# Kernel tuning notes

Measured on AMD Instinct MI355X. Metric: run time of the kernel, lower is better.

## Reference

```python
import jax, jax.numpy as jnp
import numpy as np

DIM = 1024
NUM_HEADS = 16
MASKED = True


def setup_inputs() -> dict:
    key = jax.random.key(0)
    ks = jax.random.split(key, 9)
    B, S, D = 2, 2048, DIM
    return {
        "x": jax.random.normal(ks[0], (B, S, D), dtype=jnp.float32),
        "Wq": jax.random.normal(ks[1], (D, D), dtype=jnp.float32),
        "bq": jax.random.normal(ks[2], (D,), dtype=jnp.float32),
        "Wk": jax.random.normal(ks[3], (D, D), dtype=jnp.float32),
        "bk": jax.random.normal(ks[4], (D,), dtype=jnp.float32),
        "Wv": jax.random.normal(ks[5], (D, D), dtype=jnp.float32),
        "bv": jax.random.normal(ks[6], (D,), dtype=jnp.float32),
        "Wo": jax.random.normal(ks[7], (D, D), dtype=jnp.float32),
        "bo": jax.random.normal(ks[8], (D,), dtype=jnp.float32),
    }


def _mha(x, Wq, bq, Wk, bk, Wv, bv, Wo, bo):
    B, S, D = x.shape
    H = NUM_HEADS
    hd = D // H
    # projections (torch Linear stores [out,in]; here W is [out,in], x @ W.T + b)
    q = x @ Wq.T + bq
    k = x @ Wk.T + bk
    v = x @ Wv.T + bv
    # [B, H, S, hd]
    q = q.reshape(B, S, H, hd).transpose(0, 2, 1, 3)
    k = k.reshape(B, S, H, hd).transpose(0, 2, 1, 3)
    v = v.reshape(B, S, H, hd).transpose(0, 2, 1, 3)
    scores = jnp.einsum("bhqd,bhkd->bhqk", q, k) / jnp.sqrt(jnp.asarray(hd, x.dtype))
    if MASKED:
        mask = jnp.tril(jnp.ones((S, S), dtype=bool))
        scores = jnp.where(mask, scores, -jnp.inf)
    attn = jax.nn.softmax(scores, axis=-1)
    out = jnp.einsum("bhqk,bhkd->bhqd", attn, v)
    out = out.transpose(0, 2, 1, 3).reshape(B, S, D)
    return out @ Wo.T + bo


def reference(x, Wq, bq, Wk, bk, Wv, bv, Wo, bo):
    return _mha(x, Wq, bq, Wk, bk, Wv, bv, Wo, bo)
```

## Files before the change

### kernel.cpp

```cpp
#include <hip/hip_runtime.h>

typedef unsigned short u16;
typedef unsigned int u32;
typedef __attribute__((ext_vector_type(4))) float f32x4;
typedef __attribute__((ext_vector_type(8))) __bf16 bf16x8;

#define L2E 1.4426950408889634f

__device__ __forceinline__ u16 f2bf(float f) { return __builtin_bit_cast(u16, (__bf16)f); }
__device__ __forceinline__ float bf2f(u16 h) { return (float)__builtin_bit_cast(__bf16, h); }
__device__ __forceinline__ f32x4 mfma16(bf16x8 a, bf16x8 b, f32x4 c) {
  return __builtin_amdgcn_mfma_f32_16x16x32_bf16(a, b, c, 0, 0, 0);
}
__device__ __forceinline__ void gl_lds16(const u16* g, u16* l) {
  __builtin_amdgcn_global_load_lds((__attribute__((address_space(1))) void*)g,
                                   (__attribute__((address_space(3))) void*)l,
                                   16, 0, 0);
}
__device__ __forceinline__ f32x4 fzero() {
  f32x4 v = {0.f, 0.f, 0.f, 0.f};
  return v;
}

__global__ void k_prep(const float* __restrict__ x, const float* __restrict__ Wq,
                       const float* __restrict__ Wk, const float* __restrict__ Wv,
                       const float* __restrict__ Wo,
                       u16* __restrict__ xh, u16* __restrict__ xl,
                       u16* __restrict__ wqh, u16* __restrict__ wql,
                       u16* __restrict__ wkh, u16* __restrict__ wkl,
                       u16* __restrict__ wvb, u16* __restrict__ wob) {
  int i = (blockIdx.x * 256 + threadIdx.x) * 4;
  const float* src;
  u16* hi;
  u16* lo;
  int j;
  if (i < 4194304)      { src = x;  hi = xh;  lo = xl;      j = i; }
  else if (i < 5242880) { src = Wq; hi = wqh; lo = wql;     j = i - 4194304; }
  else if (i < 6291456) { src = Wk; hi = wkh; lo = wkl;     j = i - 5242880; }
  else if (i < 7340032) { src = Wv; hi = wvb; lo = nullptr; j = i - 6291456; }
  else                  { src = Wo; hi = wob; lo = nullptr; j = i - 7340032; }
  float4 v = *(const float4*)(src + j);
  float vv[4] = {v.x, v.y, v.z, v.w};
  u16 hh[4];
#pragma unroll
  for (int t = 0; t < 4; ++t) hh[t] = f2bf(vv[t]);
  *(ushort4*)(hi + j) = make_ushort4(hh[0], hh[1], hh[2], hh[3]);
  if (lo) {
    u16 ll[4];
#pragma unroll
    for (int t = 0; t < 4; ++t) ll[t] = f2bf(vv[t] - bf2f(hh[t]));
    *(ushort4*)(lo + j) = make_ushort4(ll[0], ll[1], ll[2], ll[3]);
  }
}

template <int SPLIT, int EPI>
__device__ __forceinline__ void gemm_body(
    u16* sm, const u16* __restrict__ Ah, const u16* __restrict__ Al,
    const u16* __restrict__ Bh, const u16* __restrict__ Bl,
    const float* __restrict__ bias, float scale,
    u16* __restrict__ oH, u16* __restrict__ oL, float* __restrict__ oF,
    int m0, int n0) {
  u16* sAh = sm;
  u16* sBh = sm + 4096;
  u16* sAl = SPLIT ? (sm + 8192) : sm;
  u16* sBl = SPLIT ? (sm + 12288) : sm;

  const int tid = threadIdx.x;
  const int lane = tid & 63, w = tid >> 6;
  const int wm = w >> 1, wn = w & 1;
  const int fr = lane & 15, fg = lane >> 4;
  const int srow = tid >> 2, scb = (tid & 3) * 8;

  f32x4 acc[4][4];
#pragma unroll
  for (int i = 0; i < 4; ++i)
#pragma unroll
    for (int j = 0; j < 4; ++j) acc[i][j] = fzero();

  for (int kk = 0; kk < 1024; kk += 32) {
    __syncthreads();
#pragma unroll
    for (int r = 0; r < 2; ++r) {
      int row = r * 64 + srow;
      gl_lds16(Ah + (size_t)(m0 + row) * 1024 + kk + scb, sAh + row * 32 + scb);
      gl_lds16(Bh + (size_t)(n0 + row) * 1024 + kk + scb, sBh + row * 32 + scb);
      if constexpr (SPLIT) {
        gl_lds16(Al + (size_t)(m0 + row) * 1024 + kk + scb, sAl + row * 32 + scb);
        gl_lds16(Bl + (size_t)(n0 + row) * 1024 + kk + scb, sBl + row * 32 + scb);
      }
    }
    __syncthreads();

    bf16x8 ah[4], bh[4], al[4], bl[4];
#pragma unroll
    for (int i = 0; i < 4; ++i) {
      ah[i] = *(const bf16x8*)(sAh + (wm * 64 + i * 16 + fr) * 32 + fg * 8);
      bh[i] = *(const bf16x8*)(sBh + (wn * 64 + i * 16 + fr) * 32 + fg * 8);
      if constexpr (SPLIT) {
        al[i] = *(const bf16x8*)(sAl + (wm * 64 + i * 16 + fr) * 32 + fg * 8);
        bl[i] = *(const bf16x8*)(sBl + (wn * 64 + i * 16 + fr) * 32 + fg * 8);
      }
    }
#pragma unroll
    for (int i = 0; i < 4; ++i)
#pragma unroll
      for (int j = 0; j < 4; ++j) {
        acc[i][j] = mfma16(ah[i], bh[j], acc[i][j]);
        if constexpr (SPLIT) {
          acc[i][j] = mfma16(ah[i], bl[j], acc[i][j]);
          acc[i][j] = mfma16(al[i], bh[j], acc[i][j]);
        }
      }
  }

#pragma unroll
  for (int i = 0; i < 4; ++i)
#pragma unroll
    for (int j = 0; j < 4; ++j) {
      int cg = n0 + wn * 64 + j * 16 + fr;
      float bv = bias[cg];
#pragma unroll
      for (int r = 0; r < 4; ++r) {
        int rg = m0 + wm * 64 + i * 16 + fg * 4 + r;
        float val = (acc[i][j][r] + bv) * scale;
        if constexpr (EPI == 0) {
          int b = rg >> 11, s = rg & 2047, hd2 = cg >> 6, dd = cg & 63;
          size_t off = ((size_t)((b * 16 + hd2) * 2048 + s)) * 64 + dd;
          u16 hv = f2bf(val);
          oH[off] = hv;
          oL[off] = f2bf(val - bf2f(hv));
        } else if constexpr (EPI == 1) {
          int b = rg >> 11, s = rg & 2047, hd2 = cg >> 6, dd = cg & 63;
          size_t off = ((size_t)((b * 16 + hd2) * 64 + dd)) * 2048 + s;
          oH[off] = f2bf(val);
        } else {
          oF[(size_t)rg * 1024 + cg] = val;
        }
      }
    }
}

__global__ __launch_bounds__(256) void k_qkv(
    const u16* __restrict__ xh, const u16* __restrict__ xl,
    const u16* __restrict__ wqh, const u16* __restrict__ wql,
    const u16* __restrict__ wkh, const u16* __restrict__ wkl,
    const u16* __restrict__ wvb,
    const float* __restrict__ bq, const float* __restrict__ bk,
    const float* __restrict__ bv,
    u16* __restrict__ qh, u16* __restrict__ ql,
    u16* __restrict__ kh, u16* __restrict__ kl, u16* __restrict__ vt) {
  __shared__ u16 sm[16384];
  int which = blockIdx.y >> 3;
  int m0 = blockIdx.x * 128, n0 = (blockIdx.y & 7) * 128;
  if (which == 0)
    gemm_body<1, 0>(sm, xh, xl, wqh, wql, bq, 0.125f * L2E, qh, ql, nullptr, m0, n0);
  else if (which == 1)
    gemm_body<1, 0>(sm, xh, xl, wkh, wkl, bk, 1.0f, kh, kl, nullptr, m0, n0);
  else
    gemm_body<0, 1>(sm, xh, nullptr, wvb, nullptr, bv, 1.0f, vt, nullptr, nullptr, m0, n0);
}

__global__ __launch_bounds__(256) void k_oproj(
    const u16* __restrict__ ao, const u16* __restrict__ wob,
    const float* __restrict__ bo, float* __restrict__ out) {
  __shared__ u16 sm[8192];
  gemm_body<0, 2>(sm, ao, nullptr, wob, nullptr, bo, 1.0f, nullptr, nullptr, out,
                  blockIdx.x * 128, blockIdx.y * 128);
}

__global__ __launch_bounds__(256) void k_attn(
    const u16* __restrict__ Qh, const u16* __restrict__ Ql,
    const u16* __restrict__ Kh, const u16* __restrict__ Kl,
    const u16* __restrict__ Vt, u16* __restrict__ Oa) {
  __shared__ u16 sKh[2][4096], sKl[2][4096], sVt[2][4096];
  __shared__ u16 sP[4][1024];

  const int tid = threadIdx.x;
  const int lane = tid & 63, w = tid >> 6;
  const int fr = lane & 15, fg = lane >> 4;

  const int d = blockIdx.x;
  const int bh = (d & 7) * 4 + (d >> 7);
  const int pr = (d >> 3) & 15;

  const size_t base = (size_t)bh * 131072;
  const u16* Qh_p = Qh + base;
  const u16* Ql_p = Ql + base;
  const u16* Kh_p = Kh + base;
  const u16* Kl_p = Kl + base;
  const u16* Vt_p = Vt + base;
  const int bb = bh >> 4, hh = bh & 15;

  const int srow8 = tid >> 3, scb8 = tid & 7;

  auto STAGE = [&](int t, int c) {
#pragma unroll
    for (int r2 = 0; r2 < 2; ++r2) {
      int row = r2 * 32 + srow8;
      int cbs = scb8 ^ (row & 7);
      gl_lds16(Kh_p + ((size_t)(t * 64 + row)) * 64 + cbs * 8, &sKh[c][row * 64 + scb8 * 8]);
      gl_lds16(Kl_p + ((size_t)(t * 64 + row)) * 64 + cbs * 8, &sKl[c][row * 64 + scb8 * 8]);
      gl_lds16(Vt_p + (size_t)row * 2048 + t * 64 + cbs * 8, &sVt[c][row * 64 + scb8 * 8]);
    }
  };

  for (int half = 0; half < 2; ++half) {
    const int j = half ? (31 - pr) : pr;
    const int nt = j + 1;
    const int qrow = j * 64 + w * 16 + fr;

    bf16x8 qhf[2], qlf[2];
#pragma unroll
    for (int ks = 0; ks < 2; ++ks) {
      qhf[ks] = *(const bf16x8*)(Qh_p + (size_t)qrow * 64 + ks * 32 + fg * 8);
      qlf[ks] = *(const bf16x8*)(Ql_p + (size_t)qrow * 64 + ks * 32 + fg * 8);
    }

    float mx = -1e30f, l = 0.f;
    f32x4 o[4];
#pragma unroll
    for (int f = 0; f < 4; ++f) o[f] = fzero();

    STAGE(0, 0);

    for (int t = 0; t < nt; ++t) {
      const int cur = t & 1;
      if (t + 1 < nt) {
        STAGE(t + 1, cur ^ 1);
        asm volatile("s_waitcnt vmcnt(6)" ::: "memory");
      } else {
        asm volatile("s_waitcnt vmcnt(0)" ::: "memory");
      }
      asm volatile("s_barrier" ::: "memory");

      const u16* kbh = sKh[cur];
      const u16* kbl = sKl[cur];
      const u16* vbb = sVt[cur];

      f32x4 sc[4];
      __builtin_amdgcn_s_setprio(1);
#pragma unroll
      for (int f = 0; f < 4; ++f) {
        f32x4 a = fzero();
#pragma unroll
        for (int ks = 0; ks < 2; ++ks) {
          int row = f * 16 + fr;
          int cb = (fg + 4 * ks) ^ (fr & 7);
          bf16x8 khv = *(const bf16x8*)(kbh + row * 64 + cb * 8);
          bf16x8 klv = *(const bf16x8*)(kbl + row * 64 + cb * 8);
          a = mfma16(khv, qhf[ks], a);
          a = mfma16(khv, qlf[ks], a);
          a = mfma16(klv, qhf[ks], a);
        }
        sc[f] = a;
      }
      __builtin_amdgcn_s_setprio(0);

      if (t == nt - 1) {
#pragma unroll
        for (int f = 0; f < 4; ++f)
#pragma unroll
          for (int r = 0; r < 4; ++r) {
            int kvg = t * 64 + f * 16 + fg * 4 + r;
            if (kvg > qrow) sc[f][r] = -1e30f;
          }
      }

      float pm = -1e30f;
#pragma unroll
      for (int f = 0; f < 4; ++f)
#pragma unroll
        for (int r = 0; r < 4; ++r) pm = fmaxf(pm, sc[f][r]);
      pm = fmaxf(pm, __shfl_xor(pm, 16, 64));
      pm = fmaxf(pm, __shfl_xor(pm, 32, 64));

      const bool resc = __any(pm > mx + 11.5f);
      float alp = 1.0f;
      if (resc) {
        float mn = fmaxf(mx, pm);
        alp = exp2f(mx - mn);
        mx = mn;
      }

      float ps = 0.f;
#pragma unroll
      for (int f = 0; f < 4; ++f) {
        float p0 = exp2f(sc[f][0] - mx);
        float p1 = exp2f(sc[f][1] - mx);
        float p2 = exp2f(sc[f][2] - mx);
        float p3 = exp2f(sc[f][3] - mx);
        ps += (p0 + p1) + (p2 + p3);
        uint2 pv;
        pv.x = (u32)f2bf(p0) | ((u32)f2bf(p1) << 16);
        pv.y = (u32)f2bf(p2) | ((u32)f2bf(p3) << 16);
        int e = (f * 16 + fg * 4) ^ ((fr & 7) << 3);
        *(uint2*)(&sP[w][fr * 64 + e]) = pv;
      }
      ps += __shfl_xor(ps, 16, 64);
      ps += __shfl_xor(ps, 32, 64);
      l = l * alp + ps;

      if (resc) {
        float alpb[4];
#pragma unroll
        for (int r = 0; r < 4; ++r) alpb[r] = __shfl(alp, fg * 4 + r, 64);
#pragma unroll
        for (int f = 0; f < 4; ++f)
#pragma unroll
          for (int r = 0; r < 4; ++r) o[f][r] *= alpb[r];
      }

      __builtin_amdgcn_s_setprio(1);
#pragma unroll
      for (int ks = 0; ks < 2; ++ks) {
        int e = (ks * 32 + fg * 8) ^ ((fr & 7) << 3);
        bf16x8 pa = *(const bf16x8*)(&sP[w][fr * 64 + e]);
#pragma unroll
        for (int f = 0; f < 4; ++f) {
          int row = f * 16 + fr;
          int cb = (fg + 4 * ks) ^ (fr & 7);
          bf16x8 vb = *(const bf16x8*)(vbb + row * 64 + cb * 8);
          o[f] = mfma16(pa, vb, o[f]);
        }
      }
      __builtin_amdgcn_s_setprio(0);

      asm volatile("s_barrier" ::: "memory");
    }

    float lb[4];
#pragma unroll
    for (int r = 0; r < 4; ++r) lb[r] = __shfl(l, fg * 4 + r, 64);
#pragma unroll
    for (int f = 0; f < 4; ++f)
#pragma unroll
      for (int r = 0; r < 4; ++r) {
        int qg = j * 64 + w * 16 + fg * 4 + r;
        float val = o[f][r] / lb[r];
        Oa[((size_t)(bb * 2048 + qg)) * 1024 + hh * 64 + f * 16 + fr] = f2bf(val);
      }
  }
}

extern "C" void kernel_launch(void* const* d_in, const int* in_sizes, int n_in,
                              void* d_out, int out_size, void* d_ws, size_t ws_size,
                              hipStream_t stream) {
  const float* x  = (const float*)d_in[0];
  const float* Wq = (const float*)d_in[1];
  const float* bq = (const float*)d_in[2];
  const float* Wk = (const float*)d_in[3];
  const float* bk = (const float*)d_in[4];
  const float* Wv = (const float*)d_in[5];
  const float* bv = (const float*)d_in[6];
  const float* Wo = (const float*)d_in[7];
  const float* bo = (const float*)d_in[8];
  float* out = (float*)d_out;

  u16* ws  = (u16*)d_ws;
  u16* xh  = ws;
  u16* xl  = xh + 4194304;
  u16* wqh = xl + 4194304;
  u16* wql = wqh + 1048576;
  u16* wkh = wql + 1048576;
  u16* wkl = wkh + 1048576;
  u16* wvb = wkl + 1048576;
  u16* wob = wvb + 1048576;
  u16* qh  = wob + 1048576;
  u16* ql  = qh + 4194304;
  u16* kh  = ql + 4194304;
  u16* kl  = kh + 4194304;
  u16* vt  = kl + 4194304;
  u16* ao  = xh;

  k_prep<<<8192, 256, 0, stream>>>(x, Wq, Wk, Wv, Wo, xh, xl, wqh, wql, wkh, wkl, wvb, wob);
  k_qkv<<<dim3(32, 24), 256, 0, stream>>>(xh, xl, wqh, wql, wkh, wkl, wvb, bq, bk, bv,
                                          qh, ql, kh, kl, vt);
  k_attn<<<512, 256, 0, stream>>>(qh, ql, kh, kl, vt, ao);
  k_oproj<<<dim3(32, 8), 256, 0, stream>>>(ao, wob, bo, out);
}
```

Before: 173.0 us.

## Swizzle GEMM LDS, vectorize V store, retile oproj and widen attention blocks

The shared GEMM body now XOR-swizzles its LDS tile layout to avoid bank conflicts on fragment reads, and the V-transpose epilogue writes four bf16 values at once instead of scalar stores. The output projection gets its own 64x128 tiled kernel with more blocks. Attention moves to 512-thread blocks covering 128 query rows per block, so each staged K/V tile is shared by twice as many waves, with 256 blocks. The trade-offs are fewer attention blocks for load balancing and a mask check that now runs on the last two tiles.

Result: no change. 173.3 us (+0.2%).

```diff
diff --git a/kernel.cpp b/kernel.cpp
--- a/kernel.cpp
+++ b/kernel.cpp
@@ -69,7 +69,10 @@
   const int lane = tid & 63, w = tid >> 6;
   const int wm = w >> 1, wn = w & 1;
   const int fr = lane & 15, fg = lane >> 4;
-  const int srow = tid >> 2, scb = (tid & 3) * 8;
+  const int srow = tid >> 2, sblk = tid & 3;
+  const int sswz = (sblk ^ (srow & 3)) * 8;
+  const int sdst = sblk * 8;
+  const int rswz = (fg ^ (fr & 3)) * 8;
 
   f32x4 acc[4][4];
 #pragma unroll
@@ -82,11 +85,11 @@
 #pragma unroll
     for (int r = 0; r < 2; ++r) {
       int row = r * 64 + srow;
-      gl_lds16(Ah + (size_t)(m0 + row) * 1024 + kk + scb, sAh + row * 32 + scb);
-      gl_lds16(Bh + (size_t)(n0 + row) * 1024 + kk + scb, sBh + row * 32 + scb);
+      gl_lds16(Ah + (size_t)(m0 + row) * 1024 + kk + sswz, sAh + row * 32 + sdst);
+      gl_lds16(Bh + (size_t)(n0 + row) * 1024 + kk + sswz, sBh + row * 32 + sdst);
       if constexpr (SPLIT) {
-        gl_lds16(Al + (size_t)(m0 + row) * 1024 + kk + scb, sAl + row * 32 + scb);
-        gl_lds16(Bl + (size_t)(n0 + row) * 1024 + kk + scb, sBl + row * 32 + scb);
+        gl_lds16(Al + (size_t)(m0 + row) * 1024 + kk + sswz, sAl + row * 32 + sdst);
+        gl_lds16(Bl + (size_t)(n0 + row) * 1024 + kk + sswz, sBl + row * 32 + sdst);
       }
     }
     __syncthreads();
@@ -94,11 +97,11 @@
     bf16x8 ah[4], bh[4], al[4], bl[4];
 #pragma unroll
     for (int i = 0; i < 4; ++i) {
-      ah[i] = *(const bf16x8*)(sAh + (wm * 64 + i * 16 + fr) * 32 + fg * 8);
-      bh[i] = *(const bf16x8*)(sBh + (wn * 64 + i * 16 + fr) * 32 + fg * 8);
+      ah[i] = *(const bf16x8*)(sAh + (wm * 64 + i * 16 + fr) * 32 + rswz);
+      bh[i] = *(const bf16x8*)(sBh + (wn * 64 + i * 16 + fr) * 32 + rswz);
       if constexpr (SPLIT) {
-        al[i] = *(const bf16x8*)(sAl + (wm * 64 + i * 16 + fr) * 32 + fg * 8);
-        bl[i] = *(const bf16x8*)(sBl + (wn * 64 + i * 16 + fr) * 32 + fg * 8);
+        al[i] = *(const bf16x8*)(sAl + (wm * 64 + i * 16 + fr) * 32 + rswz);
+        bl[i] = *(const bf16x8*)(sBl + (wn * 64 + i * 16 + fr) * 32 + rswz);
       }
     }
 #pragma unroll
@@ -119,22 +122,28 @@
     for (int j = 0; j < 4; ++j) {
       int cg = n0 + wn * 64 + j * 16 + fr;
       float bv = bias[cg];
-#pragma unroll
-      for (int r = 0; r < 4; ++r) {
-        int rg = m0 + wm * 64 + i * 16 + fg * 4 + r;
-        float val = (acc[i][j][r] + bv) * scale;
-        if constexpr (EPI == 0) {
-          int b = rg >> 11, s = rg & 2047, hd2 = cg >> 6, dd = cg & 63;
-          size_t off = ((size_t)((b * 16 + hd2) * 2048 + s)) * 64 + dd;
-          u16 hv = f2bf(val);
-          oH[off] = hv;
-          oL[off] = f2bf(val - bf2f(hv));
-        } else if constexpr (EPI == 1) {
-          int b = rg >> 11, s = rg & 2047, hd2 = cg >> 6, dd = cg & 63;
-          size_t off = ((size_t)((b * 16 + hd2) * 64 + dd)) * 2048 + s;
-          oH[off] = f2bf(val);
-        } else {
-          oF[(size_t)rg * 1024 + cg] = val;
+      if constexpr (EPI == 1) {
+        int rgb = m0 + wm * 64 + i * 16 + fg * 4;
+        int b = rgb >> 11, s = rgb & 2047, hd2 = cg >> 6, dd = cg & 63;
+        u16 hv[4];
+#pragma unroll
+        for (int r = 0; r < 4; ++r) hv[r] = f2bf((acc[i][j][r] + bv) * scale);
+        *(ushort4*)(oH + ((size_t)((b * 16 + hd2) * 64 + dd)) * 2048 + s) =
+            make_ushort4(hv[0], hv[1], hv[2], hv[3]);
+      } else {
+#pragma unroll
+        for (int r = 0; r < 4; ++r) {
+          int rg = m0 + wm * 64 + i * 16 + fg * 4 + r;
+          float val = (acc[i][j][r] + bv) * scale;
+          if constexpr (EPI == 0) {
+            int b = rg >> 11, s = rg & 2047, hd2 = cg >> 6, dd = cg & 63;
+            size_t off = ((size_t)((b * 16 + hd2) * 2048 + s)) * 64 + dd;
+            u16 hv = f2bf(val);
+            oH[off] = hv;
+            oL[off] = f2bf(val - bf2f(hv));
+          } else {
+            oF[(size_t)rg * 1024 + cg] = val;
+          }
         }
       }
     }
@@ -161,27 +170,76 @@
 }
 
 __global__ __launch_bounds__(256) void k_oproj(
-    const u16* __restrict__ ao, const u16* __restrict__ wob,
-    const float* __restrict__ bo, float* __restrict__ out) {
-  __shared__ u16 sm[8192];
-  gemm_body<0, 2>(sm, ao, nullptr, wob, nullptr, bo, 1.0f, nullptr, nullptr, out,
-                  blockIdx.x * 128, blockIdx.y * 128);
-}
-
-__global__ __launch_bounds__(256) void k_attn(
+    const u16* __restrict__ A, const u16* __restrict__ B,
+    const float* __restrict__ bias, float* __restrict__ out) {
+  __shared__ u16 sm[6144];
+  u16* sA = sm;
+  u16* sB = sm + 2048;
+
+  const int tid = threadIdx.x;
+  const int lane = tid & 63, w = tid >> 6;
+  const int fr = lane & 15, fg = lane >> 4;
+  const int m0 = blockIdx.x * 64, n0 = blockIdx.y * 128;
+  const int srow = tid >> 2, sblk = tid & 3;
+  const int sswz = (sblk ^ (srow & 3)) * 8;
+  const int sdst = sblk * 8;
+  const int rswz = (fg ^ (fr & 3)) * 8;
+
+  f32x4 acc[4][2];
+#pragma unroll
+  for (int i = 0; i < 4; ++i)
+#pragma unroll
+    for (int j = 0; j < 2; ++j) acc[i][j] = fzero();
+
+  for (int kk = 0; kk < 1024; kk += 32) {
+    __syncthreads();
+    gl_lds16(A + (size_t)(m0 + srow) * 1024 + kk + sswz, sA + srow * 32 + sdst);
+    gl_lds16(B + (size_t)(n0 + srow) * 1024 + kk + sswz, sB + srow * 32 + sdst);
+    gl_lds16(B + (size_t)(n0 + 64 + srow) * 1024 + kk + sswz, sB + (64 + srow) * 32 + sdst);
+    __syncthreads();
+
+    bf16x8 af[4], bf_[2];
+#pragma unroll
+    for (int i = 0; i < 4; ++i)
+      af[i] = *(const bf16x8*)(sA + (i * 16 + fr) * 32 + rswz);
+#pragma unroll
+    for (int j = 0; j < 2; ++j)
+      bf_[j] = *(const bf16x8*)(sB + (w * 32 + j * 16 + fr) * 32 + rswz);
+#pragma unroll
+    for (int i = 0; i < 4; ++i)
+#pragma unroll
+      for (int j = 0; j < 2; ++j) acc[i][j] = mfma16(af[i], bf_[j], acc[i][j]);
+  }
+
+#pragma unroll
+  for (int i = 0; i < 4; ++i)
+#pragma unroll
+    for (int j = 0; j < 2; ++j) {
+      int cg = n0 + w * 32 + j * 16 + fr;
+      float bv = bias[cg];
+#pragma unroll
+      for (int r = 0; r < 4; ++r) {
+        int rg = m0 + i * 16 + fg * 4 + r;
+        out[(size_t)rg * 1024 + cg] = acc[i][j][r] + bv;
+      }
+    }
+}
+
+__global__ __launch_bounds__(512) void k_attn(
     const u16* __restrict__ Qh, const u16* __restrict__ Ql,
     const u16* __restrict__ Kh, const u16* __restrict__ Kl,
     const u16* __restrict__ Vt, u16* __restrict__ Oa) {
   __shared__ u16 sKh[2][4096], sKl[2][4096], sVt[2][4096];
-  __shared__ u16 sP[4][1024];
+  __shared__ u16 sP[8][1024];
 
   const int tid = threadIdx.x;
   const int lane = tid & 63, w = tid >> 6;
   const int fr = lane & 15, fg = lane >> 4;
 
   const int d = blockIdx.x;
-  const int bh = (d & 7) * 4 + (d >> 7);
-  const int pr = (d >> 3) & 15;
+  const int g = d >> 3;
+  const int bh = (d & 7) * 4 + (g & 3);
+  const int pr = g >> 2;
 
   const size_t base = (size_t)bh * 131072;
   const u16* Qh_p = Qh + base;
@@ -194,20 +252,16 @@
   const int srow8 = tid >> 3, scb8 = tid & 7;
 
   auto STAGE = [&](int t, int c) {
-#pragma unroll
-    for (int r2 = 0; r2 < 2; ++r2) {
-      int row = r2 * 32 + srow8;
-      int cbs = scb8 ^ (row & 7);
-      gl_lds16(Kh_p + ((size_t)(t * 64 + row)) * 64 + cbs * 8, &sKh[c][row * 64 + scb8 * 8]);
-      gl_lds16(Kl_p + ((size_t)(t * 64 + row)) * 64 + cbs * 8, &sKl[c][row * 64 + scb8 * 8]);
-      gl_lds16(Vt_p + (size_t)row * 2048 + t * 64 + cbs * 8, &sVt[c][row * 64 + scb8 * 8]);
-    }
+    int cbs = scb8 ^ (srow8 & 7);
+    gl_lds16(Kh_p + ((size_t)(t * 64 + srow8)) * 64 + cbs * 8, &sKh[c][srow8 * 64 + scb8 * 8]);
+    gl_lds16(Kl_p + ((size_t)(t * 64 + srow8)) * 64 + cbs * 8, &sKl[c][srow8 * 64 + scb8 * 8]);
+    gl_lds16(Vt_p + (size_t)srow8 * 2048 + t * 64 + cbs * 8, &sVt[c][srow8 * 64 + scb8 * 8]);
   };
 
   for (int half = 0; half < 2; ++half) {
-    const int j = half ? (31 - pr) : pr;
-    const int nt = j + 1;
-    const int qrow = j * 64 + w * 16 + fr;
+    const int j = half ? (15 - pr) : pr;
+    const int nt = 2 * (j + 1);
+    const int qrow = j * 128 + w * 16 + fr;
 
     bf16x8 qhf[2], qlf[2];
 #pragma unroll
@@ -227,7 +281,7 @@
       const int cur = t & 1;
       if (t + 1 < nt) {
         STAGE(t + 1, cur ^ 1);
-        asm volatile("s_waitcnt vmcnt(6)" ::: "memory");
+        asm volatile("s_waitcnt vmcnt(3)" ::: "memory");
       } else {
         asm volatile("s_waitcnt vmcnt(0)" ::: "memory");
       }
@@ -256,7 +310,7 @@
       }
       __builtin_amdgcn_s_setprio(0);
 
-      if (t == nt - 1) {
+      if (t >= nt - 2) {
 #pragma unroll
         for (int f = 0; f < 4; ++f)
 #pragma unroll
@@ -335,7 +389,7 @@
     for (int f = 0; f < 4; ++f)
 #pragma unroll
       for (int r = 0; r < 4; ++r) {
-        int qg = j * 64 + w * 16 + fg * 4 + r;
+        int qg = j * 128 + w * 16 + fg * 4 + r;
         float val = o[f][r] / lb[r];
         Oa[((size_t)(bb * 2048 + qg)) * 1024 + hh * 64 + f * 16 + fr] = f2bf(val);
       }
@@ -375,6 +429,6 @@
   k_prep<<<8192, 256, 0, stream>>>(x, Wq, Wk, Wv, Wo, xh, xl, wqh, wql, wkh, wkl, wvb, wob);
   k_qkv<<<dim3(32, 24), 256, 0, stream>>>(xh, xl, wqh, wql, wkh, wkl, wvb, bq, bk, bv,
                                           qh, ql, kh, kl, vt);
-  k_attn<<<512, 256, 0, stream>>>(qh, ql, kh, kl, vt, ao);
-  k_oproj<<<dim3(32, 8), 256, 0, stream>>>(ao, wob, bo, out);
-}
+  k_attn<<<256, 512, 0, stream>>>(qh, ql, kh, kl, vt, ao);
+  k_oproj<<<dim3(64, 8), 256, 0, stream>>>(ao, wob, bo, out);
+}
```
